# Optimization experiments

Hardware: AMD Instinct MI355X
Metric: run time of the kernel (lower is better)

Reference implementation:

```python
import jax, jax.numpy as jnp
import numpy as np

# Hyperparameters from __init__
TEMPERATURE = 0.07
HARD_POS_W = 1.5
HARD_NEG_W = 2.0
THR_POS = 0.5
THR_NEG = 0.3
NEG_LOSS_W = 0.3

B, D, N_CLASSES = 8192, 256, 1024


def setup_inputs() -> dict:
    key = jax.random.key(0)
    kf, kl = jax.random.split(key)
    features = jax.random.normal(kf, (B, D), dtype=jnp.float32)
    labels = jax.random.randint(kl, (B,), 0, N_CLASSES, dtype=jnp.int32)
    return {"features": features, "labels": labels}


def reference(features, labels):
    b = features.shape[0]
    # L2-normalize features (F.normalize(dim=1))
    anchor = features / jnp.linalg.norm(features, axis=1, keepdims=True)
    sim = anchor @ anchor.T                      # [B, B] cosine similarity
    logits = sim / TEMPERATURE
    logits = logits - jax.lax.stop_gradient(jnp.max(logits, axis=1, keepdims=True))

    mask = (labels[:, None] == labels[None, :]).astype(logits.dtype)   # same-class
    logits_mask = 1.0 - jnp.eye(b, dtype=logits.dtype)                 # exclude self

    # W2ML weights: computed from detached similarities (torch used .item())
    sim_d = jax.lax.stop_gradient(sim)
    offdiag = logits_mask > 0
    is_pos = mask > 0
    hard_pos = is_pos & (sim_d < THR_POS) & offdiag
    pos_weights = jnp.where(
        hard_pos, 1.0 + (THR_POS - sim_d) / THR_POS * (HARD_POS_W - 1.0), 1.0)
    hard_neg = (~is_pos) & (sim_d > THR_NEG) & offdiag
    neg_weights = jnp.where(
        hard_neg, 1.0 + (sim_d - THR_NEG) / (1.0 - THR_NEG) * (HARD_NEG_W - 1.0), 1.0)

    # SupCon log-prob with self excluded from the denominator
    exp_logits = jnp.exp(logits) * logits_mask
    denom = jnp.sum(exp_logits, axis=1, keepdims=True)
    log_prob = logits - jnp.log(denom)

    pos_mask = mask * logits_mask
    pos_cnt = jnp.clip(jnp.sum(pos_mask, axis=1), 1.0, None)
    positive_loss = -jnp.mean(
        jnp.sum(pos_mask * pos_weights * log_prob, axis=1) / pos_cnt)

    # Negative term: weighted mean probability mass assigned to negatives
    neg_mask = (1.0 - mask) * logits_mask
    neg_cnt = jnp.clip(jnp.sum(neg_mask, axis=1), 1.0, None)
    prob = exp_logits / denom
    negative_loss = jnp.mean(
        jnp.sum(neg_mask * neg_weights * prob, axis=1) / neg_cnt)

    return positive_loss + NEG_LOSS_W * negative_loss
```

## Files before the change

kernel.cpp:

```cpp
#include <hip/hip_runtime.h>

#define BSZ  8192
#define DDIM 256
#define BM 128
#define BN 128
#define NT   64
#define NTRI (NT * (NT + 1) / 2)

typedef float f32x4 __attribute__((ext_vector_type(4)));
typedef short bf16x8 __attribute__((ext_vector_type(8)));

__device__ __forceinline__ unsigned short f32_to_bf16(float f) {
    unsigned int u = __float_as_uint(f);
    u += 0x7fffu + ((u >> 16) & 1u);
    return (unsigned short)(u >> 16);
}

#define K_E1   20.60992915555662f
#define K_E2  -20.60992915555662f
#define K_INVT 14.285714285714286f
#define K_N1   1.4285714285714286f
#define K_N2   0.5714285714285714f

__device__ __forceinline__ void decode_tile(int t, int& It, int& Jt) {
    const int off1 = 136, off2 = 392, off3 = 648, off4 = 904, off5 = 1040,
              off6 = 1296, off7 = 1552, off8 = 1688, off9 = 1944;
    int b = (t >= off1) + (t >= off2) + (t >= off3) + (t >= off4) + (t >= off5)
          + (t >= off6) + (t >= off7) + (t >= off8) + (t >= off9);
    int si, sj, r0;
    switch (b) {
        case 0: si = 0; sj = 0; r0 = 0;    break;
        case 1: si = 0; sj = 1; r0 = off1; break;
        case 2: si = 0; sj = 2; r0 = off2; break;
        case 3: si = 0; sj = 3; r0 = off3; break;
        case 4: si = 1; sj = 1; r0 = off4; break;
        case 5: si = 1; sj = 2; r0 = off5; break;
        case 6: si = 1; sj = 3; r0 = off6; break;
        case 7: si = 2; sj = 2; r0 = off7; break;
        case 8: si = 2; sj = 3; r0 = off8; break;
        default: si = 3; sj = 3; r0 = off9; break;
    }
    const int rr = t - r0;
    int il, jl;
    if (si == sj) {
        il = 0;
        #pragma unroll
        for (int q = 1; q < 16; q++) if (rr >= (16 * q - (q * (q - 1)) / 2)) il = q;
        jl = il + (rr - (16 * il - (il * (il - 1)) / 2));
    } else {
        il = rr >> 4;
        jl = rr & 15;
    }
    It = si * 16 + il;
    Jt = sj * 16 + jl;
}

__global__ __launch_bounds__(256) void norm_kernel(const float* __restrict__ feat,
                                                   unsigned short* __restrict__ anchorT,
                                                   float* __restrict__ posAcc,
                                                   unsigned int* __restrict__ counter) {
    __shared__ __align__(16) unsigned short img[32 * 512];
    const int tid  = threadIdx.x;
    const int wid  = tid >> 6;
    const int lane = tid & 63;
    const int R0   = blockIdx.x * 64;

    posAcc[blockIdx.x * 256 + tid] = 0.0f;
    if (blockIdx.x == 0 && tid == 0) *counter = 0u;

    #pragma unroll
    for (int it = 0; it < 16; it++) {
        const int row = R0 + it * 4 + wid;
        const float4 v = ((const float4*)(feat + (size_t)row * DDIM))[lane];
        float ss = v.x * v.x + v.y * v.y + v.z * v.z + v.w * v.w;
        #pragma unroll
        for (int off = 32; off > 0; off >>= 1) ss += __shfl_xor(ss, off, 64);
        const float inv = rsqrtf(ss);
        ushort4 o;
        o.x = f32_to_bf16(v.x * inv);
        o.y = f32_to_bf16(v.y * inv);
        o.z = f32_to_bf16(v.z * inv);
        o.w = f32_to_bf16(v.w * inv);
        const int C    = lane >> 3;
        const int c    = C * 4 + ((row >> 4) & 3);
        const int l16  = (row & 15) + (((lane >> 1) & 3) << 4);
        *(ushort4*)(&img[c * 512 + l16 * 8 + (lane & 1) * 4]) = o;
    }
    __syncthreads();
    #pragma unroll
    for (int p = 0; p < 8; p++) {
        const int c = p * 4 + wid;
        const int T = (c >> 2) * 512 + (R0 >> 4) + (c & 3);
        *(bf16x8*)(anchorT + (size_t)T * 512 + lane * 8) = *(const bf16x8*)(&img[c * 512 + lane * 8]);
    }
}

__device__ __forceinline__ void gload_lds16(const unsigned short* g, unsigned short* l) {
    __builtin_amdgcn_global_load_lds(
        (const __attribute__((address_space(1))) void*)g,
        (__attribute__((address_space(3))) void*)l, 16, 0, 0);
}

__global__ __launch_bounds__(512) void simloss_kernel(
    const unsigned short* __restrict__ anchorT,
    const int* __restrict__ labels,
    float* __restrict__ part,
    float* __restrict__ posAcc)
{
    __shared__ __align__(16) unsigned short As[8 * 512];
    __shared__ __align__(16) unsigned short As2[8 * 512];
    __shared__ __align__(16) unsigned short Bs[8 * 512];
    __shared__ __align__(16) unsigned short Bs2[8 * 512];
    __shared__ float rowDT[2][BM][2];
    __shared__ float colDT[4][BN][2];
    __shared__ int rowLab[BM];
    __shared__ int colLab[BN];

    int It, Jt;
    decode_tile(blockIdx.x, It, Jt);
    const bool diag = (It == Jt);
    const int I0 = It * BM, J0 = Jt * BN;

    const int tid  = threadIdx.x;
    const int lane = tid & 63;
    const int w    = tid >> 6;
    const int rw   = w >> 1;
    const int cw   = w & 1;
    const int cl   = lane & 15;
    const int rg   = lane >> 4;
    const int laneOff = lane * 8;

    if (tid < BM) rowLab[tid] = labels[I0 + tid];
    else if (tid < 2 * BM) colLab[tid - BM] = labels[J0 + tid - BM];

    f32x4 acc[2][4];
    #pragma unroll
    for (int f = 0; f < 2; f++)
        #pragma unroll
        for (int g = 0; g < 4; g++)
            acc[f][g] = (f32x4){0.f, 0.f, 0.f, 0.f};

    #pragma unroll
    for (int kc = 0; kc < 4; kc++) {
        {
            const int C0 = kc * 2;
            const size_t ga0 = ((size_t)C0 * 512 + It * 8) * 512;
            const size_t gb0 = ((size_t)C0 * 512 + Jt * 8) * 512;
            const size_t ga1 = ((size_t)(C0 + 1) * 512 + It * 8) * 512;
            const size_t gb1 = ((size_t)(C0 + 1) * 512 + Jt * 8) * 512;
            gload_lds16(anchorT + ga0 + tid * 8, &As[w * 512]);
            gload_lds16(anchorT + gb0 + tid * 8, &Bs[w * 512]);
            gload_lds16(anchorT + ga1 + tid * 8, &As2[w * 512]);
            gload_lds16(anchorT + gb1 + tid * 8, &Bs2[w * 512]);
        }
        __syncthreads();
        #pragma unroll
        for (int ks = 0; ks < 2; ks++) {
            const unsigned short* aB = (ks == 0 ? As : As2) + (rw * 2) * 512 + laneOff;
            const unsigned short* bB = (ks == 0 ? Bs : Bs2) + (cw * 4) * 512 + laneOff;
            const bf16x8 a0 = *(const bf16x8*)(aB);
            const bf16x8 a1 = *(const bf16x8*)(aB + 512);
            const bf16x8 b0 = *(const bf16x8*)(bB);
            const bf16x8 b1 = *(const bf16x8*)(bB + 512);
            const bf16x8 b2 = *(const bf16x8*)(bB + 1024);
            const bf16x8 b3 = *(const bf16x8*)(bB + 1536);
            acc[0][0] = __builtin_amdgcn_mfma_f32_16x16x32_bf16(a0, b0, acc[0][0], 0, 0, 0);
            acc[0][1] = __builtin_amdgcn_mfma_f32_16x16x32_bf16(a0, b1, acc[0][1], 0, 0, 0);
            acc[0][2] = __builtin_amdgcn_mfma_f32_16x16x32_bf16(a0, b2, acc[0][2], 0, 0, 0);
            acc[0][3] = __builtin_amdgcn_mfma_f32_16x16x32_bf16(a0, b3, acc[0][3], 0, 0, 0);
            acc[1][0] = __builtin_amdgcn_mfma_f32_16x16x32_bf16(a1, b0, acc[1][0], 0, 0, 0);
            acc[1][1] = __builtin_amdgcn_mfma_f32_16x16x32_bf16(a1, b1, acc[1][1], 0, 0, 0);
            acc[1][2] = __builtin_amdgcn_mfma_f32_16x16x32_bf16(a1, b2, acc[1][2], 0, 0, 0);
            acc[1][3] = __builtin_amdgcn_mfma_f32_16x16x32_bf16(a1, b3, acc[1][3], 0, 0, 0);
        }
        __syncthreads();
    }

    int ljr[4], gjr[4];
    #pragma unroll
    for (int g = 0; g < 4; g++) {
        const int cidx = cw * 64 + g * 16 + cl;
        ljr[g] = colLab[cidx];
        gjr[g] = J0 + cidx;
    }
    float cd[4] = {0.f, 0.f, 0.f, 0.f}, ct[4] = {0.f, 0.f, 0.f, 0.f};

    #pragma unroll
    for (int f = 0; f < 2; f++) {
        float rd[4] = {0.f, 0.f, 0.f, 0.f}, rt[4] = {0.f, 0.f, 0.f, 0.f};
        int li[4], gi[4];
        #pragma unroll
        for (int r = 0; r < 4; r++) {
            const int ridx = rw * 32 + f * 16 + rg * 4 + r;
            li[r] = rowLab[ridx];
            gi[r] = I0 + ridx;
        }
        #pragma unroll
        for (int g = 0; g < 4; g++) {
            const int lj = ljr[g];
            const bool granule = (rw * 2 + f) == (cw * 4 + g);
            const f32x4 c = acc[f][g];
            #pragma unroll
            for (int r = 0; r < 4; r++) {
                const float s = c[r];
                const bool self = diag && granule && ((rg * 4 + r) == cl);
                const float e  = self ? 0.f : exp2f(fmaf(s, K_E1, K_E2));
                const float wn = fmaxf(fmaf(s, K_N1, K_N2), 1.0f);
                const float we = wn * e;
                rd[r] += e;  rt[r] += we;
                if (!diag) { cd[g] += e; ct[g] += we; }
                if (li[r] == lj && !self) {
                    const float wp = fmaxf(1.5f - s, 1.0f);
                    const float slp = fmaf(s, K_INVT, -K_INVT) * wp;
                    float* pi = posAcc + (size_t)gi[r] * 4;
                    atomicAdd(pi + 0, slp);
                    atomicAdd(pi + 1, wp);
                    atomicAdd(pi + 2, we);
                    atomicAdd(pi + 3, 1.0f);
                    if (!diag) {
                        float* pj = posAcc + (size_t)gjr[g] * 4;
                        atomicAdd(pj + 0, slp);
                        atomicAdd(pj + 1, wp);
                        atomicAdd(pj + 2, we);
                        atomicAdd(pj + 3, 1.0f);
                    }
                }
            }
        }
        #pragma unroll
        for (int r = 0; r < 4; r++) {
            #pragma unroll
            for (int off = 1; off < 16; off <<= 1) {
                rd[r] += __shfl_xor(rd[r], off, 64);
                rt[r] += __shfl_xor(rt[r], off, 64);
            }
        }
        if (cl == 0) {
            #pragma unroll
            for (int r = 0; r < 4; r++) {
                const int row = rw * 32 + f * 16 + rg * 4 + r;
                rowDT[cw][row][0] = rd[r];
                rowDT[cw][row][1] = rt[r];
            }
        }
    }
    if (!diag) {
        #pragma unroll
        for (int g = 0; g < 4; g++) {
            cd[g] += __shfl_xor(cd[g], 16, 64);
            cd[g] += __shfl_xor(cd[g], 32, 64);
            ct[g] += __shfl_xor(ct[g], 16, 64);
            ct[g] += __shfl_xor(ct[g], 32, 64);
        }
        if (rg == 0) {
            #pragma unroll
            for (int g = 0; g < 4; g++) {
                const int col = cw * 64 + g * 16 + cl;
                colDT[rw][col][0] = cd[g];
                colDT[rw][col][1] = ct[g];
            }
        }
    }

    __syncthreads();
    if (tid < BM) {
        float2 v;
        v.x = rowDT[0][tid][0] + rowDT[1][tid][0];
        v.y = rowDT[0][tid][1] + rowDT[1][tid][1];
        ((float2*)part)[(size_t)Jt * BSZ + I0 + tid] = v;
    } else if (tid < 2 * BM && !diag) {
        const int c = tid - BM;
        float2 v;
        v.x = colDT[0][c][0] + colDT[1][c][0] + colDT[2][c][0] + colDT[3][c][0];
        v.y = colDT[0][c][1] + colDT[1][c][1] + colDT[2][c][1] + colDT[3][c][1];
        ((float2*)part)[(size_t)It * BSZ + J0 + c] = v;
    }
}

__global__ __launch_bounds__(256) void reduce_final_kernel(
    const float* __restrict__ part, const float* __restrict__ posAcc,
    double* __restrict__ partial, unsigned int* __restrict__ counter,
    float* __restrict__ out)
{
    const int i = blockIdx.x * 256 + threadIdx.x;
    float dsum = 0.f, T2 = 0.f;
    const float2* p2 = (const float2*)part;
    #pragma unroll 8
    for (int j = 0; j < NT; j++) {
        const float2 v = p2[(size_t)j * BSZ + i];
        dsum += v.x; T2 += v.y;
    }
    const float4 pa = ((const float4*)posAcc)[i];
    const float s1 = pa.x, w1 = pa.y, s2 = T2 - pa.z, cnt = pa.w;
    const float pc = fmaxf(cnt, 1.0f);
    const float nc = fmaxf(8191.0f - cnt, 1.0f);
    const float ld = logf(dsum);
    const double pos_i = (double)((s1 - ld * w1) / pc);
    const double neg_i = (double)((s2 / dsum) / nc);

    __shared__ double sp[256], sn[256];
    sp[threadIdx.x] = pos_i; sn[threadIdx.x] = neg_i;
    __syncthreads();
    for (int s = 128; s > 0; s >>= 1) {
        if (threadIdx.x < s) {
            sp[threadIdx.x] += sp[threadIdx.x + s];
            sn[threadIdx.x] += sn[threadIdx.x + s];
        }
        __syncthreads();
    }
    __shared__ bool amLast;
    if (threadIdx.x == 0) {
        partial[blockIdx.x * 2 + 0] = sp[0];
        partial[blockIdx.x * 2 + 1] = sn[0];
        __threadfence();
        amLast = (atomicAdd(counter, 1u) == 31u);
    }
    __syncthreads();
    if (amLast) {
        __threadfence();
        const int lane = threadIdx.x;
        double p = 0.0, n = 0.0;
        if (lane < 32) {
            volatile double* vp = (volatile double*)partial;
            p = vp[lane * 2 + 0];
            n = vp[lane * 2 + 1];
        }
        #pragma unroll
        for (int o = 32; o > 0; o >>= 1) { p += __shfl_xor(p, o, 64); n += __shfl_xor(n, o, 64); }
        if (lane == 0) out[0] = (float)(-p / (double)BSZ + 0.3 * (n / (double)BSZ));
    }
}

extern "C" void kernel_launch(void* const* d_in, const int* in_sizes, int n_in,
                              void* d_out, int out_size, void* d_ws, size_t ws_size,
                              hipStream_t stream) {
    const float* feat = (const float*)d_in[0];
    const int* labels = (const int*)d_in[1];
    float* out = (float*)d_out;

    char* ws = (char*)d_ws;
    unsigned short* anchorT = (unsigned short*)ws;
    const size_t anchorBytes = (size_t)BSZ * DDIM * sizeof(unsigned short);
    float* part = (float*)(ws + anchorBytes);
    const size_t partBytes = (size_t)NT * BSZ * 2 * sizeof(float);
    float* posAcc = (float*)(ws + anchorBytes + partBytes);
    const size_t posBytes = (size_t)BSZ * 4 * sizeof(float);
    double* partial = (double*)(ws + anchorBytes + partBytes + posBytes);
    unsigned int* counter = (unsigned int*)(ws + anchorBytes + partBytes + posBytes + 512);

    norm_kernel<<<BSZ / 64, 256, 0, stream>>>(feat, anchorT, posAcc, counter);
    simloss_kernel<<<NTRI, 512, 0, stream>>>(anchorT, labels, part, posAcc);
    reduce_final_kernel<<<BSZ / 256, 256, 0, stream>>>(part, posAcc, partial, counter, out);
}
```

Baseline: 117.3 us.

## Raise grid parallelism in norm and reduce kernels, use hardware exp2

The norm kernel now handles 16 rows per block instead of 64, which quadruples the grid, and it writes each row group directly into the tiled layout. The reduce kernel splits each row's 64 partial columns across 8 lanes and combines them with shuffles, running 256 blocks instead of 32. The loss kernel's exp2f is replaced by the raw v_exp_f32 instruction, which skips the range-handling wrapper. Together these aim to fill more CUs in the small kernels and shorten the hot exponential, at the cost of a larger final 256-way reduction and possibly slightly different exp accuracy.

```diff
diff --git a/kernel.cpp b/kernel.cpp
--- a/kernel.cpp
+++ b/kernel.cpp
@@ -15,6 +15,16 @@
     u += 0x7fffu + ((u >> 16) & 1u);
     return (unsigned short)(u >> 16);
 }
+
+#if __has_builtin(__builtin_amdgcn_exp2f)
+__device__ __forceinline__ float fast_exp2(float x) { return __builtin_amdgcn_exp2f(x); }
+#else
+__device__ __forceinline__ float fast_exp2(float x) {
+    float r;
+    asm("v_exp_f32 %0, %1" : "=v"(r) : "v"(x));
+    return r;
+}
+#endif
 
 #define K_E1   20.60992915555662f
 #define K_E2  -20.60992915555662f
@@ -59,17 +69,18 @@
                                                    unsigned short* __restrict__ anchorT,
                                                    float* __restrict__ posAcc,
                                                    unsigned int* __restrict__ counter) {
-    __shared__ __align__(16) unsigned short img[32 * 512];
+    __shared__ __align__(16) unsigned short img[8 * 512];
     const int tid  = threadIdx.x;
     const int wid  = tid >> 6;
     const int lane = tid & 63;
-    const int R0   = blockIdx.x * 64;
-
-    posAcc[blockIdx.x * 256 + tid] = 0.0f;
+    const int R    = blockIdx.x;
+    const int R0   = R * 16;
+
+    if (tid < 64) posAcc[blockIdx.x * 64 + tid] = 0.0f;
     if (blockIdx.x == 0 && tid == 0) *counter = 0u;
 
     #pragma unroll
-    for (int it = 0; it < 16; it++) {
+    for (int it = 0; it < 4; it++) {
         const int row = R0 + it * 4 + wid;
         const float4 v = ((const float4*)(feat + (size_t)row * DDIM))[lane];
         float ss = v.x * v.x + v.y * v.y + v.z * v.z + v.w * v.w;
@@ -82,16 +93,15 @@
         o.z = f32_to_bf16(v.z * inv);
         o.w = f32_to_bf16(v.w * inv);
         const int C    = lane >> 3;
-        const int c    = C * 4 + ((row >> 4) & 3);
         const int l16  = (row & 15) + (((lane >> 1) & 3) << 4);
-        *(ushort4*)(&img[c * 512 + l16 * 8 + (lane & 1) * 4]) = o;
+        *(ushort4*)(&img[C * 512 + l16 * 8 + (lane & 1) * 4]) = o;
     }
     __syncthreads();
     #pragma unroll
-    for (int p = 0; p < 8; p++) {
+    for (int p = 0; p < 2; p++) {
         const int c = p * 4 + wid;
-        const int T = (c >> 2) * 512 + (R0 >> 4) + (c & 3);
-        *(bf16x8*)(anchorT + (size_t)T * 512 + lane * 8) = *(const bf16x8*)(&img[c * 512 + lane * 8]);
+        *(bf16x8*)(anchorT + ((size_t)(c * 512 + R)) * 512 + lane * 8) =
+            *(const bf16x8*)(&img[c * 512 + lane * 8]);
     }
 }
 
@@ -204,7 +214,7 @@
             for (int r = 0; r < 4; r++) {
                 const float s = c[r];
                 const bool self = diag && granule && ((rg * 4 + r) == cl);
-                const float e  = self ? 0.f : exp2f(fmaf(s, K_E1, K_E2));
+                const float e  = self ? 0.f : fast_exp2(fmaf(s, K_E1, K_E2));
                 const float wn = fmaxf(fmaf(s, K_N1, K_N2), 1.0f);
                 const float we = wn * e;
                 rd[r] += e;  rt[r] += we;
@@ -282,52 +292,60 @@
     double* __restrict__ partial, unsigned int* __restrict__ counter,
     float* __restrict__ out)
 {
-    const int i = blockIdx.x * 256 + threadIdx.x;
+    const int t   = threadIdx.x;
+    const int row = blockIdx.x * 32 + (t >> 3);
+    const int sg  = t & 7;
     float dsum = 0.f, T2 = 0.f;
     const float2* p2 = (const float2*)part;
-    #pragma unroll 8
-    for (int j = 0; j < NT; j++) {
-        const float2 v = p2[(size_t)j * BSZ + i];
+    #pragma unroll
+    for (int j = 0; j < 8; j++) {
+        const float2 v = p2[(size_t)(sg * 8 + j) * BSZ + row];
         dsum += v.x; T2 += v.y;
     }
-    const float4 pa = ((const float4*)posAcc)[i];
-    const float s1 = pa.x, w1 = pa.y, s2 = T2 - pa.z, cnt = pa.w;
-    const float pc = fmaxf(cnt, 1.0f);
-    const float nc = fmaxf(8191.0f - cnt, 1.0f);
-    const float ld = logf(dsum);
-    const double pos_i = (double)((s1 - ld * w1) / pc);
-    const double neg_i = (double)((s2 / dsum) / nc);
-
-    __shared__ double sp[256], sn[256];
-    sp[threadIdx.x] = pos_i; sn[threadIdx.x] = neg_i;
+    #pragma unroll
+    for (int off = 1; off < 8; off <<= 1) {
+        dsum += __shfl_xor(dsum, off, 64);
+        T2   += __shfl_xor(T2,   off, 64);
+    }
+    __shared__ double sp[32], sn[32];
+    if (sg == 0) {
+        const float4 pa = ((const float4*)posAcc)[row];
+        const float s1 = pa.x, w1 = pa.y, s2 = T2 - pa.z, cnt = pa.w;
+        const float pc = fmaxf(cnt, 1.0f);
+        const float nc = fmaxf(8191.0f - cnt, 1.0f);
+        const float ld = logf(dsum);
+        sp[t >> 3] = (double)((s1 - ld * w1) / pc);
+        sn[t >> 3] = (double)((s2 / dsum) / nc);
+    }
     __syncthreads();
-    for (int s = 128; s > 0; s >>= 1) {
-        if (threadIdx.x < s) {
-            sp[threadIdx.x] += sp[threadIdx.x + s];
-            sn[threadIdx.x] += sn[threadIdx.x + s];
-        }
-        __syncthreads();
-    }
     __shared__ bool amLast;
-    if (threadIdx.x == 0) {
-        partial[blockIdx.x * 2 + 0] = sp[0];
-        partial[blockIdx.x * 2 + 1] = sn[0];
-        __threadfence();
-        amLast = (atomicAdd(counter, 1u) == 31u);
+    if (t < 32) {
+        double p = sp[t], n = sn[t];
+        #pragma unroll
+        for (int off = 1; off < 32; off <<= 1) {
+            p += __shfl_xor(p, off, 64);
+            n += __shfl_xor(n, off, 64);
+        }
+        if (t == 0) {
+            partial[blockIdx.x * 2 + 0] = p;
+            partial[blockIdx.x * 2 + 1] = n;
+            __threadfence();
+            amLast = (atomicAdd(counter, 1u) == 255u);
+        }
     }
     __syncthreads();
     if (amLast) {
         __threadfence();
-        const int lane = threadIdx.x;
-        double p = 0.0, n = 0.0;
-        if (lane < 32) {
-            volatile double* vp = (volatile double*)partial;
-            p = vp[lane * 2 + 0];
-            n = vp[lane * 2 + 1];
-        }
-        #pragma unroll
-        for (int o = 32; o > 0; o >>= 1) { p += __shfl_xor(p, o, 64); n += __shfl_xor(n, o, 64); }
-        if (lane == 0) out[0] = (float)(-p / (double)BSZ + 0.3 * (n / (double)BSZ));
+        __shared__ double fp[256], fn[256];
+        volatile double* vp = (volatile double*)partial;
+        fp[t] = vp[t * 2 + 0];
+        fn[t] = vp[t * 2 + 1];
+        __syncthreads();
+        for (int s = 128; s > 0; s >>= 1) {
+            if (t < s) { fp[t] += fp[t + s]; fn[t] += fn[t + s]; }
+            __syncthreads();
+        }
+        if (t == 0) out[0] = (float)(-fp[0] / (double)BSZ + 0.3 * (fn[0] / (double)BSZ));
     }
 }
 
@@ -346,9 +364,9 @@
     float* posAcc = (float*)(ws + anchorBytes + partBytes);
     const size_t posBytes = (size_t)BSZ * 4 * sizeof(float);
     double* partial = (double*)(ws + anchorBytes + partBytes + posBytes);
-    unsigned int* counter = (unsigned int*)(ws + anchorBytes + partBytes + posBytes + 512);
-
-    norm_kernel<<<BSZ / 64, 256, 0, stream>>>(feat, anchorT, posAcc, counter);
+    unsigned int* counter = (unsigned int*)(ws + anchorBytes + partBytes + posBytes + 4096);
+
+    norm_kernel<<<BSZ / 16, 256, 0, stream>>>(feat, anchorT, posAcc, counter);
     simloss_kernel<<<NTRI, 512, 0, stream>>>(anchorT, labels, part, posAcc);
-    reduce_final_kernel<<<BSZ / 256, 256, 0, stream>>>(part, posAcc, partial, counter, out);
-}
+    reduce_final_kernel<<<BSZ / 32, 256, 0, stream>>>(part, posAcc, partial, counter, out);
+}
```

New measurement: 117.2 us, median of 2. Within noise of the previous version (-0.1%).
